# Optimization experiments

Measured on AMD Instinct MI355X. Metric: run time of the kernel, lower is better.

## Reference

```python
import jax, jax.numpy as jnp
import numpy as np

T = 128        # number of time points
D = 64         # flattened state dim (bs * z_dim, bs = 1)
H = 256        # hidden width of f-network
HK = 128       # hidden width of kernel network
MAX_IT = 3     # fixed-point iterations (args.max_iterations)


def setup_inputs() -> dict:
    key = jax.random.key(0)
    ks = jax.random.split(key, 6)
    g = lambda k, sh, sc: (jax.random.normal(k, sh, jnp.float32) * sc)
    z0 = jax.random.normal(ks[0], (1, D), jnp.float32)
    t = jnp.linspace(0.0, 1.0, T, dtype=jnp.float32)
    # f: D -> H -> D MLP (the 'func' integrand network)
    W1 = g(ks[1], (D, H), 1.0 / np.sqrt(D)); b1 = jnp.zeros((H,), jnp.float32)
    W2 = g(ks[2], (H, D), 1.0 / np.sqrt(H)); b2 = jnp.zeros((D,), jnp.float32)
    # kernel: (x, s) -> D*D matrix entries (the neural kernel K)
    Wk1 = g(ks[3], (2, HK), 1.0 / np.sqrt(2.0)); bk1 = jnp.zeros((HK,), jnp.float32)
    Wk2 = g(ks[4], (HK, D * D), 1.0 / np.sqrt(HK)); bk2 = jnp.zeros((D * D,), jnp.float32)
    return dict(z0=z0, t=t, W1=W1, b1=b1, W2=W2, b2=b2,
                Wk1=Wk1, bk1=bk1, Wk2=Wk2, bk2=bk2)


def _trapezoid_weights(t):
    """w[i, j]: trapezoid quadrature weight of node j for integral over [t0, t_i]."""
    dt = t[1] - t[0]  # uniform grid
    idx = jnp.arange(T)
    mask = (idx[None, :] <= idx[:, None]).astype(t.dtype)
    w = dt * mask
    w = w.at[(idx, idx)].multiply(0.5)   # halve right endpoint of each row
    w = w.at[:, 0].multiply(0.5)         # halve left endpoint
    w = w.at[0].set(0.0)                 # zero-length integral at t0
    return w


def _solve(z0, t, W1, b1, W2, b2, Wk1, bk1, Wk2, bk2):
    y0 = z0.reshape(-1)                                   # [D], solver flattens batch
    w = _trapezoid_weights(t)                             # [T, T]
    # Neural kernel K(x_i, s_j) -> [D, D], precomputed once on the grid.
    pairs = jnp.stack([jnp.broadcast_to(t[:, None], (T, T)),
                       jnp.broadcast_to(t[None, :], (T, T))], axis=-1)  # [T, T, 2]
    hK = jnp.tanh(pairs @ Wk1 + bk1)                      # [T, T, HK]
    K = (hK @ Wk2 + bk2).reshape(T, T, D, D)              # [T, T, D, D]

    def f(y):  # integrand network, applied over all time points
        return jnp.tanh(y @ W1 + b1) @ W2 + b2            # [T, D]

    def step(y, _):
        # G_i = \int_0^{x_i} K(x_i, s) f(y(s)) ds  (trapezoid on grid)
        G = jnp.einsum('ij,ijde,je->id', w, K, f(y))      # [T, D]
        # y'(x) = G(x)  =>  y_i = y0 + \int_0^{x_i} G(s) ds
        y_new = y0[None, :] + w @ G                       # [T, D]
        return y_new, None

    y_init = jnp.tile(y0[None, :], (T, 1))                # fixed-point initial guess
    y, _ = jax.lax.scan(step, y_init, None, length=MAX_IT)
    return y


def reference(z0, t, W1, b1, W2, b2, Wk1, bk1, Wk2, bk2):
    y = _solve(z0, t, W1, b1, W2, b2, Wk1, bk1, Wk2, bk2)  # [T, D]
    return y[-1].reshape(1, D)  # z[-1]: final state, shape [bs, dim]
```

## Files before the change

### kernel.cpp

```cpp
#include <hip/hip_runtime.h>
#include <hip/hip_bf16.h>

#define TT 128
#define DD 64
#define HH 256
#define HK 128
#define JH (TT*HK)
#define HD (HK*DD)
#define NCHUNK 64

__global__ void __launch_bounds__(256)
k_F0M0(const float* __restrict__ z0,
       const float* __restrict__ W1, const float* __restrict__ b1,
       const float* __restrict__ W2, const float* __restrict__ b2,
       const float* __restrict__ bk2, const float* __restrict__ Wk2,
       float* __restrict__ M0, float* __restrict__ bF0) {
    int bx = blockIdx.x, tid = threadIdx.x;
    int part = tid >> 6, d = tid & 63;
    __shared__ float red[4][64];
    __shared__ float ys[DD];
    __shared__ float hs[HH];
    __shared__ __attribute__((aligned(16))) float fs[DD];
    if (tid < DD) ys[tid] = z0[tid];
    __syncthreads();
    float acc = b1[tid];
    #pragma unroll 8
    for (int e = 0; e < DD; ++e) acc += ys[e] * W1[e * HH + tid];
    hs[tid] = tanhf(acc);
    __syncthreads();
    {
        float s = 0.f;
        #pragma unroll 8
        for (int h = part * 64; h < part * 64 + 64; ++h) s += hs[h] * W2[h * DD + d];
        red[part][d] = s;
    }
    __syncthreads();
    if (part == 0)
        fs[d] = b2[d] + red[0][d] + red[1][d] + red[2][d] + red[3][d];
    __syncthreads();
    if (bx == 0) {
        float s = 0.f;
        #pragma unroll
        for (int e = part * 16; e < part * 16 + 16; ++e) s += bk2[d * DD + e] * fs[e];
        red[part][d] = s;
        __syncthreads();
        if (part == 0)
            bF0[d] = red[0][d] + red[1][d] + red[2][d] + red[3][d];
    }
    int hd = bx * 256 + tid;
    const float* Wrow = Wk2 + (size_t)(hd >> 6) * (DD * DD) + (size_t)(hd & 63) * DD;
    float a = 0.f;
    #pragma unroll
    for (int e = 0; e < DD; e += 8) {
        float4 wa = *(const float4*)(Wrow + e);
        float4 wb = *(const float4*)(Wrow + e + 4);
        float4 fa = *(const float4*)&fs[e];
        float4 fb = *(const float4*)&fs[e + 4];
        a += fa.x*wa.x + fa.y*wa.y + fa.z*wa.z + fa.w*wa.w
           + fb.x*wb.x + fb.y*wb.y + fb.z*wb.z + fb.w*wb.w;
    }
    M0[hd] = a;
}

__global__ void __launch_bounds__(256)
k_G0(const float* __restrict__ t, const float* __restrict__ Wk1,
     const float* __restrict__ bk1, const float* __restrict__ M0,
     const float* __restrict__ bF0, float* __restrict__ G) {
    int i = blockIdx.x, tid = threadIdx.x;
    int part = tid >> 6, d = tid & 63;
    __shared__ float Bpart[2][HK];
    __shared__ float Bs[HK];
    __shared__ float red[4][64];
    float dt = t[1] - t[0];
    int h = tid & 127, half = tid >> 7;
    float b = 0.f;
    if (i > 0) {
        float wk0 = Wk1[h], wk1v = Wk1[HK + h], bk = bk1[h];
        float ti = t[i];
        for (int j = half; j <= i; j += 2) {
            float w = dt * ((j == 0 || j == i) ? 0.5f : 1.0f);
            b += w * tanhf(ti * wk0 + t[j] * wk1v + bk);
        }
    }
    Bpart[half][h] = b;
    __syncthreads();
    if (tid < HK) Bs[tid] = Bpart[0][tid] + Bpart[1][tid];
    __syncthreads();
    float a = 0.f;
    #pragma unroll 8
    for (int h2 = part * 32; h2 < part * 32 + 32; ++h2)
        a += Bs[h2] * M0[h2 * DD + d];
    red[part][d] = a;
    __syncthreads();
    if (part == 0) {
        float g = red[0][d] + red[1][d] + red[2][d] + red[3][d];
        if (i > 0) g += dt * (float)i * bF0[d];
        G[i * DD + d] = g;
    }
}

__global__ void __launch_bounds__(256)
k_F(const float* __restrict__ G, const float* __restrict__ z0,
    const float* __restrict__ t,
    const float* __restrict__ W1, const float* __restrict__ b1,
    const float* __restrict__ W2, const float* __restrict__ b2,
    const float* __restrict__ bk2,
    float* __restrict__ F, float* __restrict__ bF) {
    int j = blockIdx.x, tid = threadIdx.x;
    int part = tid >> 6, d = tid & 63;
    __shared__ float red[4][64];
    __shared__ float ys[DD];
    __shared__ float hs[HH];
    __shared__ float fs[DD];
    float dt = t[1] - t[0];
    {
        float s = 0.f;
        if (j > 0) {
            for (int jp = part; jp <= j; jp += 4) {
                float w = (jp == 0 || jp == j) ? 0.5f : 1.0f;
                s += w * G[jp * DD + d];
            }
        }
        red[part][d] = s;
        __syncthreads();
        if (part == 0)
            ys[d] = z0[d] + dt * (red[0][d] + red[1][d] + red[2][d] + red[3][d]);
    }
    __syncthreads();
    float acc = b1[tid];
    #pragma unroll 8
    for (int e = 0; e < DD; ++e) acc += ys[e] * W1[e * HH + tid];
    hs[tid] = tanhf(acc);
    __syncthreads();
    {
        float s = 0.f;
        #pragma unroll 8
        for (int h = part * 64; h < part * 64 + 64; ++h) s += hs[h] * W2[h * DD + d];
        red[part][d] = s;
    }
    __syncthreads();
    if (part == 0) {
        float a = b2[d] + red[0][d] + red[1][d] + red[2][d] + red[3][d];
        fs[d] = a;
        F[j * DD + d] = a;
    }
    __syncthreads();
    {
        float s = 0.f;
        #pragma unroll
        for (int e = part * 16; e < part * 16 + 16; ++e) s += bk2[d * DD + e] * fs[e];
        red[part][d] = s;
    }
    __syncthreads();
    if (part == 0)
        bF[j * DD + d] = red[0][d] + red[1][d] + red[2][d] + red[3][d];
}

__global__ void __launch_bounds__(256)
k_M(const float* __restrict__ F, const float* __restrict__ Wk2,
    float* __restrict__ M) {
    int tid = threadIdx.x;
    int hd = blockIdx.x * 256 + tid;
    int j0 = blockIdx.y * 8;
    __shared__ __attribute__((aligned(16))) float Fs[8][64];
    for (int k = tid; k < 8 * DD; k += 256) Fs[k >> 6][k & 63] = F[j0 * DD + k];
    __syncthreads();
    float acc[8] = {0.f,0.f,0.f,0.f,0.f,0.f,0.f,0.f};
    const float* Wrow = Wk2 + (size_t)(hd >> 6) * (DD * DD) + (size_t)(hd & 63) * DD;
    for (int e = 0; e < DD; e += 8) {
        float4 wa = *(const float4*)(Wrow + e);
        float4 wb = *(const float4*)(Wrow + e + 4);
        #pragma unroll
        for (int r = 0; r < 8; ++r) {
            float4 f0 = *(const float4*)&Fs[r][e];
            float4 f1 = *(const float4*)&Fs[r][e + 4];
            acc[r] += f0.x*wa.x + f0.y*wa.y + f0.z*wa.z + f0.w*wa.w
                    + f1.x*wb.x + f1.y*wb.y + f1.z*wb.z + f1.w*wb.w;
        }
    }
    #pragma unroll
    for (int r = 0; r < 8; ++r) M[(size_t)(j0 + r) * HD + hd] = acc[r];
}

__global__ void __launch_bounds__(256)
k_G1(const float* __restrict__ t, const float* __restrict__ Wk1,
     const float* __restrict__ bk1, const float* __restrict__ M,
     float* __restrict__ P, const float* __restrict__ z0,
     float* __restrict__ out, int final_it) {
    int itile = blockIdx.x, c = blockIdx.y;
    if (c > 4 * itile + 3) return;
    __shared__ __attribute__((aligned(16))) float As[8 * 256];
    __shared__ float red[4][8][64];
    int tid = threadIdx.x, sub = tid >> 6, d = tid & 63;

    {
        float dt = t[1] - t[0];
        int h = tid & 127;
        int j = 2 * c + (tid >> 7);
        float wk0 = Wk1[h], wk1v = Wk1[HK + h], bk = bk1[h];
        float tj = t[j];
        #pragma unroll
        for (int k = 0; k < 8; ++k) {
            int i = itile * 8 + k;
            float w = (i == 0 || j > i) ? 0.f : dt * ((j == 0 || j == i) ? 0.5f : 1.0f);
            As[k * 256 + tid] = w * tanhf(t[i] * wk0 + tj * wk1v + bk);
        }
    }
    if (final_it && itile == 0 && c == 0 && tid < DD) out[tid] = z0[tid];
    __syncthreads();

    float acc[8] = {0.f,0.f,0.f,0.f,0.f,0.f,0.f,0.f};
    const float* Mp = M + ((size_t)c * 256) * DD + d;
    int jl0 = sub * 64;
    for (int jl = jl0; jl < jl0 + 64; jl += 8) {
        float m0 = Mp[(size_t)(jl + 0) * DD];
        float m1 = Mp[(size_t)(jl + 1) * DD];
        float m2 = Mp[(size_t)(jl + 2) * DD];
        float m3 = Mp[(size_t)(jl + 3) * DD];
        float m4 = Mp[(size_t)(jl + 4) * DD];
        float m5 = Mp[(size_t)(jl + 5) * DD];
        float m6 = Mp[(size_t)(jl + 6) * DD];
        float m7 = Mp[(size_t)(jl + 7) * DD];
        #pragma unroll
        for (int r = 0; r < 8; ++r) {
            float4 a0 = *(const float4*)&As[r * 256 + jl];
            float4 a1 = *(const float4*)&As[r * 256 + jl + 4];
            acc[r] += a0.x*m0 + a0.y*m1 + a0.z*m2 + a0.w*m3
                    + a1.x*m4 + a1.y*m5 + a1.z*m6 + a1.w*m7;
        }
    }
    #pragma unroll
    for (int r = 0; r < 8; ++r) red[sub][r][d] = acc[r];
    __syncthreads();
    if (sub == 0) {
        #pragma unroll
        for (int r = 0; r < 8; ++r) {
            float v = red[0][r][d] + red[1][r][d] + red[2][r][d] + red[3][r][d];
            P[(size_t)c * (TT * DD) + (itile * 8 + r) * DD + d] = v;
        }
    }
}

__global__ void __launch_bounds__(256)
k_Gfin(const float* __restrict__ P, const float* __restrict__ bF,
       const float* __restrict__ t, float* __restrict__ G,
       float* __restrict__ out, int final_it) {
    int j = blockIdx.x, tid = threadIdx.x;
    int part = tid >> 6, d = tid & 63;
    __shared__ float red[4][64];
    float dt = t[1] - t[0];
    float a = 0.f;
    int cmax = j >> 1;
    for (int c = part; c <= cmax; c += 4) a += P[(size_t)c * (TT * DD) + j * DD + d];
    if (j > 0) {
        float s = 0.f;
        for (int jp = part; jp <= j; jp += 4) {
            float w = (jp == 0 || jp == j) ? 0.5f : 1.0f;
            s += w * bF[jp * DD + d];
        }
        a += dt * s;
    }
    red[part][d] = a;
    __syncthreads();
    if (part == 0) {
        float v = red[0][d] + red[1][d] + red[2][d] + red[3][d];
        G[j * DD + d] = v;
        if (final_it) {
            float wj = (j == 0 || j == TT - 1) ? 0.5f : 1.0f;
            atomicAdd(&out[d], dt * wj * v);
        }
    }
}

extern "C" void kernel_launch(void* const* d_in, const int* in_sizes, int n_in,
                              void* d_out, int out_size, void* d_ws, size_t ws_size,
                              hipStream_t stream) {
    const float* z0  = (const float*)d_in[0];
    const float* t   = (const float*)d_in[1];
    const float* W1  = (const float*)d_in[2];
    const float* b1  = (const float*)d_in[3];
    const float* W2  = (const float*)d_in[4];
    const float* b2  = (const float*)d_in[5];
    const float* Wk1 = (const float*)d_in[6];
    const float* bk1 = (const float*)d_in[7];
    const float* Wk2 = (const float*)d_in[8];
    const float* bk2 = (const float*)d_in[9];
    float* out = (float*)d_out;

    float* ws  = (float*)d_ws;
    float* M   = ws;
    float* F   = M   + (size_t)TT*HK*DD;
    float* bF  = F   + TT*DD;
    float* G   = bF  + TT*DD;
    float* P   = G   + TT*DD;
    float* M0  = P   + (size_t)NCHUNK*TT*DD;
    float* bF0 = M0  + HD;

    k_F0M0<<<32, 256, 0, stream>>>(z0, W1, b1, W2, b2, bk2, Wk2, M0, bF0);
    k_G0<<<TT, 256, 0, stream>>>(t, Wk1, bk1, M0, bF0, G);
    for (int it = 1; it < 3; ++it) {
        int fin = (it == 2) ? 1 : 0;
        k_F<<<TT, 256, 0, stream>>>(G, z0, t, W1, b1, W2, b2, bk2, F, bF);
        k_M<<<dim3(32, 16), 256, 0, stream>>>(F, Wk2, M);
        k_G1<<<dim3(16, NCHUNK), 256, 0, stream>>>(t, Wk1, bk1, M, P, z0, out, fin);
        k_Gfin<<<TT, 256, 0, stream>>>(P, bF, t, G, out, fin);
    }
}
```

Baseline: 186.1 us.

## Fuse f-network evaluation into M contraction kernel with 8-row batching

Merges k_F and k_M into one kernel, k_FM. Each block recomputes y, the f MLP and F for 8 time points and then contracts F against its share of Wk2 to write M. This removes one launch per iteration and the F round trip through global memory. The prefix sum over G is batched per 8 rows, and W1/W2 loads are shared across those rows. The cost is that the MLP is recomputed redundantly in each of 16 hd-chunk blocks, and the grid shrinks from 512 to 256 blocks.

```diff
diff --git a/kernel.cpp b/kernel.cpp
--- a/kernel.cpp
+++ b/kernel.cpp
@@ -100,86 +100,124 @@
 }
 
 __global__ void __launch_bounds__(256)
-k_F(const float* __restrict__ G, const float* __restrict__ z0,
-    const float* __restrict__ t,
-    const float* __restrict__ W1, const float* __restrict__ b1,
-    const float* __restrict__ W2, const float* __restrict__ b2,
-    const float* __restrict__ bk2,
-    float* __restrict__ F, float* __restrict__ bF) {
-    int j = blockIdx.x, tid = threadIdx.x;
-    int part = tid >> 6, d = tid & 63;
-    __shared__ float red[4][64];
-    __shared__ float ys[DD];
-    __shared__ float hs[HH];
-    __shared__ float fs[DD];
+k_FM(const float* __restrict__ G, const float* __restrict__ z0,
+     const float* __restrict__ t,
+     const float* __restrict__ W1, const float* __restrict__ b1,
+     const float* __restrict__ W2, const float* __restrict__ b2,
+     const float* __restrict__ bk2, const float* __restrict__ Wk2,
+     float* __restrict__ M, float* __restrict__ bF) {
+    int hc = blockIdx.x;
+    int j0 = blockIdx.y * 8;
+    int tid = threadIdx.x, part = tid >> 6, d = tid & 63;
+    __shared__ float ys[8][DD];
+    __shared__ float hs[8][HH];
+    __shared__ float red[4][8][DD];
+    __shared__ __attribute__((aligned(16))) float Fs[8][DD];
     float dt = t[1] - t[0];
+
     {
         float s = 0.f;
-        if (j > 0) {
-            for (int jp = part; jp <= j; jp += 4) {
-                float w = (jp == 0 || jp == j) ? 0.5f : 1.0f;
-                s += w * G[jp * DD + d];
+        for (int p = 1 + part; p < j0; p += 4) s += G[p * DD + d];
+        red[part][0][d] = s;
+    }
+    __syncthreads();
+    if (part == 0) {
+        float S = red[0][0][d] + red[1][0][d] + red[2][0][d] + red[3][0][d];
+        float g0 = G[d];
+        float gr[8];
+        #pragma unroll
+        for (int r = 0; r < 8; ++r) gr[r] = G[(j0 + r) * DD + d];
+        float base = z0[d];
+        float run = S;
+        #pragma unroll
+        for (int r = 0; r < 8; ++r) {
+            int j = j0 + r;
+            if (j == 0) {
+                ys[r][d] = base;
+            } else {
+                ys[r][d] = base + dt * (0.5f * g0 + run + 0.5f * gr[r]);
+                run += gr[r];
             }
         }
-        red[part][d] = s;
+    }
+    __syncthreads();
+
+    float acc[8];
+    {
+        float bb = b1[tid];
+        #pragma unroll
+        for (int r = 0; r < 8; ++r) acc[r] = bb;
+    }
+    #pragma unroll 8
+    for (int e = 0; e < DD; ++e) {
+        float w1v = W1[e * HH + tid];
+        #pragma unroll
+        for (int r = 0; r < 8; ++r) acc[r] += ys[r][e] * w1v;
+    }
+    #pragma unroll
+    for (int r = 0; r < 8; ++r) hs[r][tid] = tanhf(acc[r]);
+    __syncthreads();
+
+    {
+        float a2[8] = {0.f,0.f,0.f,0.f,0.f,0.f,0.f,0.f};
+        #pragma unroll 8
+        for (int h = part * 64; h < part * 64 + 64; ++h) {
+            float w2v = W2[h * DD + d];
+            #pragma unroll
+            for (int r = 0; r < 8; ++r) a2[r] += hs[r][h] * w2v;
+        }
+        #pragma unroll
+        for (int r = 0; r < 8; ++r) red[part][r][d] = a2[r];
+    }
+    __syncthreads();
+    {
+        #pragma unroll
+        for (int rr = 0; rr < 2; ++rr) {
+            int r = part * 2 + rr;
+            Fs[r][d] = b2[d] + red[0][r][d] + red[1][r][d] +
+                       red[2][r][d] + red[3][r][d];
+        }
+    }
+    __syncthreads();
+
+    if (hc == 0) {
+        float a3[8] = {0.f,0.f,0.f,0.f,0.f,0.f,0.f,0.f};
+        for (int e = part * 16; e < part * 16 + 16; ++e) {
+            float bv = bk2[d * DD + e];
+            #pragma unroll
+            for (int r = 0; r < 8; ++r) a3[r] += Fs[r][e] * bv;
+        }
+        #pragma unroll
+        for (int r = 0; r < 8; ++r) red[part][r][d] = a3[r];
         __syncthreads();
-        if (part == 0)
-            ys[d] = z0[d] + dt * (red[0][d] + red[1][d] + red[2][d] + red[3][d]);
-    }
-    __syncthreads();
-    float acc = b1[tid];
-    #pragma unroll 8
-    for (int e = 0; e < DD; ++e) acc += ys[e] * W1[e * HH + tid];
-    hs[tid] = tanhf(acc);
-    __syncthreads();
-    {
-        float s = 0.f;
-        #pragma unroll 8
-        for (int h = part * 64; h < part * 64 + 64; ++h) s += hs[h] * W2[h * DD + d];
-        red[part][d] = s;
-    }
-    __syncthreads();
-    if (part == 0) {
-        float a = b2[d] + red[0][d] + red[1][d] + red[2][d] + red[3][d];
-        fs[d] = a;
-        F[j * DD + d] = a;
-    }
-    __syncthreads();
-    {
-        float s = 0.f;
-        #pragma unroll
-        for (int e = part * 16; e < part * 16 + 16; ++e) s += bk2[d * DD + e] * fs[e];
-        red[part][d] = s;
-    }
-    __syncthreads();
-    if (part == 0)
-        bF[j * DD + d] = red[0][d] + red[1][d] + red[2][d] + red[3][d];
-}
-
-__global__ void __launch_bounds__(256)
-k_M(const float* __restrict__ F, const float* __restrict__ Wk2,
-    float* __restrict__ M) {
-    int tid = threadIdx.x;
-    int hd = blockIdx.x * 256 + tid;
-    int j0 = blockIdx.y * 8;
-    __shared__ __attribute__((aligned(16))) float Fs[8][64];
-    for (int k = tid; k < 8 * DD; k += 256) Fs[k >> 6][k & 63] = F[j0 * DD + k];
-    __syncthreads();
-    float acc[8] = {0.f,0.f,0.f,0.f,0.f,0.f,0.f,0.f};
-    const float* Wrow = Wk2 + (size_t)(hd >> 6) * (DD * DD) + (size_t)(hd & 63) * DD;
-    for (int e = 0; e < DD; e += 8) {
-        float4 wa = *(const float4*)(Wrow + e);
-        float4 wb = *(const float4*)(Wrow + e + 4);
-        #pragma unroll
-        for (int r = 0; r < 8; ++r) {
-            float4 f0 = *(const float4*)&Fs[r][e];
-            float4 f1 = *(const float4*)&Fs[r][e + 4];
-            acc[r] += f0.x*wa.x + f0.y*wa.y + f0.z*wa.z + f0.w*wa.w
-                    + f1.x*wb.x + f1.y*wb.y + f1.z*wb.z + f1.w*wb.w;
-        }
-    }
+        #pragma unroll
+        for (int rr = 0; rr < 2; ++rr) {
+            int r = part * 2 + rr;
+            bF[(j0 + r) * DD + d] = red[0][r][d] + red[1][r][d] +
+                                    red[2][r][d] + red[3][r][d];
+        }
+    }
+
     #pragma unroll
-    for (int r = 0; r < 8; ++r) M[(size_t)(j0 + r) * HD + hd] = acc[r];
+    for (int q = 0; q < 2; ++q) {
+        int hd = hc * 512 + q * 256 + tid;
+        const float* Wrow = Wk2 + (size_t)(hd >> 6) * (DD * DD) + (size_t)(hd & 63) * DD;
+        float m[8] = {0.f,0.f,0.f,0.f,0.f,0.f,0.f,0.f};
+        #pragma unroll
+        for (int e = 0; e < DD; e += 8) {
+            float4 wa = *(const float4*)(Wrow + e);
+            float4 wb = *(const float4*)(Wrow + e + 4);
+            #pragma unroll
+            for (int r = 0; r < 8; ++r) {
+                float4 fa = *(const float4*)&Fs[r][e];
+                float4 fb = *(const float4*)&Fs[r][e + 4];
+                m[r] += fa.x*wa.x + fa.y*wa.y + fa.z*wa.z + fa.w*wa.w
+                      + fb.x*wb.x + fb.y*wb.y + fb.z*wb.z + fb.w*wb.w;
+            }
+        }
+        #pragma unroll
+        for (int r = 0; r < 8; ++r) M[(size_t)(j0 + r) * HD + hd] = m[r];
+    }
 }
 
 __global__ void __launch_bounds__(256)
@@ -289,8 +327,7 @@
 
     float* ws  = (float*)d_ws;
     float* M   = ws;
-    float* F   = M   + (size_t)TT*HK*DD;
-    float* bF  = F   + TT*DD;
+    float* bF  = M   + (size_t)TT*HK*DD;
     float* G   = bF  + TT*DD;
     float* P   = G   + TT*DD;
     float* M0  = P   + (size_t)NCHUNK*TT*DD;
@@ -300,8 +337,8 @@
     k_G0<<<TT, 256, 0, stream>>>(t, Wk1, bk1, M0, bF0, G);
     for (int it = 1; it < 3; ++it) {
         int fin = (it == 2) ? 1 : 0;
-        k_F<<<TT, 256, 0, stream>>>(G, z0, t, W1, b1, W2, b2, bk2, F, bF);
-        k_M<<<dim3(32, 16), 256, 0, stream>>>(F, Wk2, M);
+        k_FM<<<dim3(16, 16), 256, 0, stream>>>(G, z0, t, W1, b1, W2, b2,
+                                               bk2, Wk2, M, bF);
         k_G1<<<dim3(16, NCHUNK), 256, 0, stream>>>(t, Wk1, bk1, M, P, z0, out, fin);
         k_Gfin<<<TT, 256, 0, stream>>>(P, bF, t, G, out, fin);
     }
```

New measurement: 189.6 us. About the same (+1.9%).
